# Kernel optimization log

Measured on AMD Instinct MI355X. Metric: run time of the kernel, lower is better.

Reference implementation:

```python
import jax, jax.numpy as jnp
import numpy as np
from jax import lax

DIM = 384; D_STATE = 16; D_CONV = 4; EXPAND = 2
D_INNER = DIM * EXPAND            # 768
DT_RANK = (DIM + 15) // 16        # 24
B_, H_, W_, Z_ = 2, 16, 16, 16
L_ = H_ * W_ * Z_                 # 4096 tokens
NSL = 16                          # num_slices_small

def silu(v):
    return v * jax.nn.sigmoid(v)

def setup_inputs() -> dict:
    keys = iter(jax.random.split(jax.random.key(0), 64))
    def rnd(shape, s=0.02):
        return jax.random.normal(next(keys), shape, jnp.float32) * s
    inp = {"x": jax.random.normal(next(keys), (B_, DIM, H_, W_, Z_), jnp.float32)}
    inp["ln_g"] = jnp.ones((DIM,), jnp.float32); inp["ln_b"] = jnp.zeros((DIM,), jnp.float32)
    inp["in_w"] = rnd((2 * D_INNER, DIM)); inp["out_w"] = rnd((DIM, D_INNER))
    # standard S4D-real init: A_log = log([1..d_state]) per inner channel
    A0 = jnp.log(jnp.tile(jnp.arange(1, D_STATE + 1, dtype=jnp.float32), (D_INNER, 1)))
    for t in ("f", "b", "s"):   # forward / backward / slice-wise scan branches
        inp["convw_" + t] = rnd((D_INNER, 1, D_CONV), 0.1)
        inp["convb_" + t] = jnp.zeros((D_INNER,), jnp.float32)
        inp["xpw_" + t] = rnd((DT_RANK + 2 * D_STATE, D_INNER))
        inp["dtw_" + t] = rnd((D_INNER, DT_RANK), 0.1)
        inp["dtb_" + t] = jnp.full((D_INNER,), -4.6, jnp.float32)  # softplus ~= 0.01
        inp["Alog_" + t] = A0
        inp["Dp_" + t] = jnp.ones((D_INNER,), jnp.float32)
    for i in (1, 2, 3, 4):      # FeatureFusion3D 1x1x1 convs == channel GEMMs
        inp["c%dw" % i] = rnd((DIM, DIM)); inp["c%db" % i] = jnp.zeros((DIM,), jnp.float32)
    return inp

def _ssm_scan(dt, Bc, Cc, u, A, Dp):
    # dt,u: [B,L,di]; Bc,Cc: [B,L,ds]; A: [di,ds]  -- selective scan, time-major lax.scan
    def step(h, inp):
        dt_t, B_t, C_t, u_t = inp                      # [B,di],[B,ds],[B,ds],[B,di]
        h = h * jnp.exp(dt_t[..., None] * A) + (dt_t * u_t)[..., None] * B_t[:, None, :]
        return h, jnp.einsum('bds,bs->bd', h, C_t)
    xs = (dt.swapaxes(0, 1), Bc.swapaxes(0, 1), Cc.swapaxes(0, 1), u.swapaxes(0, 1))
    h0 = jnp.zeros((dt.shape[0], A.shape[0], A.shape[1]), dt.dtype)
    _, ys = lax.scan(step, h0, xs)                     # ys: [L,B,di]
    return ys.swapaxes(0, 1) + u * Dp

def _branch(xi, convw, convb, xpw, dtw, dtb, Alog, Dp):
    # xi: [B,L,di]; causal depthwise conv1d + SiLU, then input-dependent dt/B/C, then scan
    xc = lax.conv_general_dilated(xi.swapaxes(1, 2), convw, (1,), [(D_CONV - 1, 0)],
                                  feature_group_count=D_INNER,
                                  dimension_numbers=('NCH', 'OIH', 'NCH'))
    xc = silu((xc + convb[None, :, None]).swapaxes(1, 2))      # [B,L,di]
    dbl = xc @ xpw.T                                           # [B,L,dt_rank+2*ds]
    dt_r, Bc, Cc = jnp.split(dbl, [DT_RANK, DT_RANK + D_STATE], axis=-1)
    dt = jax.nn.softplus(dt_r @ dtw.T + dtb)                   # [B,L,di]
    return _ssm_scan(dt, Bc, Cc, xc, -jnp.exp(Alog), Dp)

def _forward(x, ln_g, ln_b, in_w, out_w,
             convw_f, convb_f, xpw_f, dtw_f, dtb_f, Alog_f, Dp_f,
             convw_b, convb_b, xpw_b, dtw_b, dtb_b, Alog_b, Dp_b,
             convw_s, convb_s, xpw_s, dtw_s, dtb_s, Alog_s, Dp_s,
             c1w, c1b, c2w, c2b, c3w, c3b, c4w, c4b):
    B, C = x.shape[:2]; img = x.shape[2:]; L = img[0] * img[1] * img[2]
    xf = x.reshape(B, C, L).swapaxes(1, 2)                     # [B,L,C]
    mu = xf.mean(-1, keepdims=True)
    var = xf.var(-1, keepdims=True)
    xn = (xf - mu) * lax.rsqrt(var + 1e-5) * ln_g + ln_b       # LayerNorm
    xz = xn @ in_w.T                                           # [B,L,2*di]
    xi, z = jnp.split(xz, 2, axis=-1)
    # slice-wise reordering for the v3 inter-slice scan (static permutation)
    perm = np.arange(L).reshape(NSL, L // NSL).T.reshape(-1)
    inv = np.argsort(perm)
    y_f = _branch(xi, convw_f, convb_f, xpw_f, dtw_f, dtb_f, Alog_f, Dp_f)
    y_b = jnp.flip(_branch(jnp.flip(xi, 1), convw_b, convb_b, xpw_b, dtw_b, dtb_b, Alog_b, Dp_b), 1)
    y_s = _branch(xi[:, perm], convw_s, convb_s, xpw_s, dtw_s, dtb_s, Alog_s, Dp_s)[:, inv]
    g = silu(z)
    x_sq = ((y_f + y_b) * g) @ out_w.T                         # bidirectional branch output
    x_sl = (y_s * g) @ out_w.T                                 # slice-scan branch output
    out_sq = x_sq.swapaxes(1, 2).reshape(B, C, *img)
    out_sl = x_sl.swapaxes(1, 2).reshape(B, C, *img)
    out = out_sq + out_sl
    # FeatureFusion3D: global branch (avgpool + two 1x1x1) + spatial branch (two 1x1x1)
    gp = out.mean(axis=(2, 3, 4))                              # [B,C]
    gf = jax.nn.relu(gp @ c1w.T + c1b) @ c2w.T + c2b
    sp = jax.nn.relu(jnp.einsum('oc,bcxyz->boxyz', c3w, out) + c3b[None, :, None, None, None])
    sp = jnp.einsum('oc,bcxyz->boxyz', c4w, sp) + c4b[None, :, None, None, None]
    wff = jax.nn.sigmoid(gf[:, :, None, None, None] + sp)
    return out_sq * wff + (1.0 - wff) * out_sl + x             # gated combine + residual

def reference(x, ln_g, ln_b, in_w, out_w,
              convw_f, convb_f, xpw_f, dtw_f, dtb_f, Alog_f, Dp_f,
              convw_b, convb_b, xpw_b, dtw_b, dtb_b, Alog_b, Dp_b,
              convw_s, convb_s, xpw_s, dtw_s, dtb_s, Alog_s, Dp_s,
              c1w, c1b, c2w, c2b, c3w, c3b, c4w, c4b):
    return _forward(x, ln_g, ln_b, in_w, out_w,
                    convw_f, convb_f, xpw_f, dtw_f, dtb_f, Alog_f, Dp_f,
                    convw_b, convb_b, xpw_b, dtw_b, dtb_b, Alog_b, Dp_b,
                    convw_s, convb_s, xpw_s, dtw_s, dtb_s, Alog_s, Dp_s,
                    c1w, c1b, c2w, c2b, c3w, c3b, c4w, c4b)
```

## Files before the change

kernel.cpp:

```cpp
#include <hip/hip_runtime.h>
#include <math.h>

#define LT     4096
#define CDIM   384
#define DI     768
#define DS     16
#define NBATCH 2
#define NCHK   128
#define CHSZ   32
#define NSUP   16
#define MROWS  (NBATCH*LT)
#define NPROJ  800

using short8 = __attribute__((ext_vector_type(8))) short;
using f32x4  = __attribute__((ext_vector_type(4))) float;

__device__ __forceinline__ int posmap(int branch, int t){
  if (branch == 0) return t;
  if (branch == 1) return LT - 1 - t;
  return ((t & 15) << 8) | (t >> 4);
}

__device__ __forceinline__ short f2bf(float f){
  union { float f; unsigned u; } v; v.f = f;
  unsigned r = (v.u + 0x7FFFu + ((v.u >> 16) & 1u)) >> 16;
  return (short)r;
}
__device__ __forceinline__ float bf2f(short s){
  union { unsigned u; float f; } v; v.u = ((unsigned)(unsigned short)s) << 16;
  return v.f;
}
__device__ __forceinline__ float softplusf(float x){
  return (x > 20.f) ? x : __logf(1.f + __expf(x));
}

__global__ __launch_bounds__(256) void cvt_bf16(const float* __restrict__ src,
    short* __restrict__ dst, int n)
{
  const int i = blockIdx.x*256 + threadIdx.x;
  if (i < n) dst[i] = f2bf(src[i]);
}

#define LNPAD 69
__global__ __launch_bounds__(256) void ln_kernel(const float* __restrict__ x,
    const float* __restrict__ gam, const float* __restrict__ bet,
    short* __restrict__ xn)
{
  __shared__ float tile[64 * LNPAD];
  __shared__ float redS[16][16][4];
  __shared__ float redS2[16][16][4];
  __shared__ float muL[64], rsL[64];
  const int b  = blockIdx.y;
  const int l0 = blockIdx.x * 64;
  const int t  = threadIdx.x;
  const int g  = t >> 4, lf = t & 15;
  float s[4] = {0,0,0,0}, s2[4] = {0,0,0,0};
  for (int cc = 0; cc < 24; cc++){
    const int c = cc*16 + g;
    const float4 v = *(const float4*)&x[((size_t)b*CDIM + c)*LT + l0 + lf*4];
    s[0]+=v.x; s[1]+=v.y; s[2]+=v.z; s[3]+=v.w;
    s2[0]+=v.x*v.x; s2[1]+=v.y*v.y; s2[2]+=v.z*v.z; s2[3]+=v.w*v.w;
  }
#pragma unroll
  for (int j = 0; j < 4; j++){ redS[g][lf][j] = s[j]; redS2[g][lf][j] = s2[j]; }
  __syncthreads();
  if (t < 64){
    float ss = 0.f, ss2 = 0.f;
#pragma unroll
    for (int gg = 0; gg < 16; gg++){
      ss  += redS[gg][t>>2][t&3];
      ss2 += redS2[gg][t>>2][t&3];
    }
    const float mu  = ss * (1.f/CDIM);
    const float var = ss2 * (1.f/CDIM) - mu*mu;
    muL[t] = mu; rsL[t] = rsqrtf(var + 1e-5f);
  }
  __syncthreads();
  for (int chunk = 0; chunk < 6; chunk++){
    const int c0 = chunk*64;
#pragma unroll
    for (int p = 0; p < 4; p++){
      const int cl = p*16 + g;
      const float4 v = *(const float4*)&x[((size_t)b*CDIM + c0 + cl)*LT + l0 + lf*4];
      tile[cl*LNPAD + lf*4 + 0] = v.x;
      tile[cl*LNPAD + lf*4 + 1] = v.y;
      tile[cl*LNPAD + lf*4 + 2] = v.z;
      tile[cl*LNPAD + lf*4 + 3] = v.w;
    }
    __syncthreads();
    const int c_w = t & 63;
    const float gv = gam[c0 + c_w], bv = bet[c0 + c_w];
#pragma unroll
    for (int p = 0; p < 16; p++){
      const int l = p*4 + (t >> 6);
      xn[((size_t)b*LT + l0 + l)*CDIM + c0 + c_w] =
          f2bf((tile[c_w*LNPAD + l] - muL[l])*rsL[l]*gv + bv);
    }
    __syncthreads();
  }
}

__global__ __launch_bounds__(256) void mkwcat(const float* __restrict__ xpw,
    const float* __restrict__ dtw, short* __restrict__ wcat)
{
  const int k = blockIdx.x*256 + threadIdx.x;
  const int o = blockIdx.y;
  if (o < 32){
    wcat[(size_t)o*DI + k] = f2bf(xpw[(size_t)(24 + o)*DI + k]);
  } else {
    const float* dr = dtw + (size_t)(o - 32)*24;
    float acc = 0.f;
#pragma unroll
    for (int j = 0; j < 24; j++) acc += dr[j] * xpw[(size_t)j*DI + k];
    wcat[(size_t)o*DI + k] = f2bf(acc);
  }
}

template<int ACT>
__global__ __launch_bounds__(256) void gemm_bf16(const short* __restrict__ A, int lda,
    const short* __restrict__ Bw, int ldb, const float* __restrict__ bias,
    void* __restrict__ C, void* __restrict__ C2, int ldc,
    int M, int N, int K)
{
  __shared__ __align__(16) short As[64*40];
  __shared__ __align__(16) short Bs[64*40];
  const int tid  = threadIdx.x;
  const int m0   = blockIdx.x*64, n0 = blockIdx.y*64;
  const int w    = tid >> 6, lane = tid & 63;
  const int wm   = (w >> 1)*32, wn = (w & 1)*32;
  const int lrow = lane & 15, lko = (lane >> 4)*8;
  const int lr   = tid >> 2, lkc = (tid & 3)*8;

  const short* Aptr = A + (size_t)(m0 + lr)*lda + lkc;
  const bool   bok  = (n0 + lr) < N;
  const short* Bptr = Bw + (size_t)(n0 + lr)*ldb + lkc;

  f32x4 acc[2][2];
#pragma unroll
  for (int i = 0; i < 2; i++)
#pragma unroll
    for (int j = 0; j < 2; j++) acc[i][j] = (f32x4){0.f,0.f,0.f,0.f};

  short8 pa = *(const short8*)Aptr;
  short8 pb = bok ? *(const short8*)Bptr : (short8){0,0,0,0,0,0,0,0};

  for (int k0 = 0; k0 < K; k0 += 32){
    *(short8*)&As[lr*40 + lkc] = pa;
    *(short8*)&Bs[lr*40 + lkc] = pb;
    __syncthreads();
    if (k0 + 32 < K){
      pa = *(const short8*)(Aptr + k0 + 32);
      pb = bok ? *(const short8*)(Bptr + k0 + 32) : (short8){0,0,0,0,0,0,0,0};
    }
    const short8 a0 = *(const short8*)&As[(wm +      lrow)*40 + lko];
    const short8 a1 = *(const short8*)&As[(wm + 16 + lrow)*40 + lko];
    const short8 b0 = *(const short8*)&Bs[(wn +      lrow)*40 + lko];
    const short8 b1 = *(const short8*)&Bs[(wn + 16 + lrow)*40 + lko];
    acc[0][0] = __builtin_amdgcn_mfma_f32_16x16x32_bf16(a0, b0, acc[0][0], 0,0,0);
    acc[0][1] = __builtin_amdgcn_mfma_f32_16x16x32_bf16(a0, b1, acc[0][1], 0,0,0);
    acc[1][0] = __builtin_amdgcn_mfma_f32_16x16x32_bf16(a1, b0, acc[1][0], 0,0,0);
    acc[1][1] = __builtin_amdgcn_mfma_f32_16x16x32_bf16(a1, b1, acc[1][1], 0,0,0);
    __syncthreads();
  }
#pragma unroll
  for (int mi = 0; mi < 2; mi++){
#pragma unroll
    for (int nj = 0; nj < 2; nj++){
      const int n = n0 + wn + nj*16 + lrow;
      if (n >= N) continue;
      const float bv = ((ACT == 0 || ACT == 8 || ACT == 9) && bias) ? bias[n] : 0.f;
#pragma unroll
      for (int reg = 0; reg < 4; reg++){
        const int m = m0 + wm + mi*16 + (lane >> 4)*4 + reg;
        float v = acc[mi][nj][reg] + bv;
        if (ACT == 0){
          ((float*)C)[(size_t)m*ldc + n] = v;
        } else if (ACT == 4){
          if (n < DI) ((short*)C)[(size_t)m*DI + n] = f2bf(v);
          else ((short*)C2)[(size_t)m*DI + (n - DI)] = f2bf(v / (1.f + __expf(-v)));
        } else if (ACT == 6){
          if (n < 32) ((float*)C)[(size_t)m*32 + n] = v;
          else ((short*)C2)[(size_t)m*DI + (n - 32)] =
                   f2bf(softplusf(v + bias[n - 32]));
        } else if (ACT == 7){
          ((short*)C)[(size_t)m*ldc + n] = f2bf(v);
        } else if (ACT == 8){
          ((short*)C)[(size_t)m*ldc + n] = f2bf(fmaxf(v, 0.f));
        } else if (ACT == 9){
          ((short*)C)[(size_t)m*ldc + n] = f2bf(v);
        }
      }
    }
  }
}

__global__ __launch_bounds__(256) void conv_branch(const short* __restrict__ xi,
    const float* __restrict__ w, const float* __restrict__ bias,
    short* __restrict__ xc, int branch)
{
  const int d  = blockIdx.x*256 + threadIdx.x;
  const int t0 = blockIdx.y*4;
  const int b  = blockIdx.z;
  const float w0 = w[d*4+0], w1 = w[d*4+1], w2 = w[d*4+2], w3 = w[d*4+3];
  const float bv = bias[d];
  float xm3 = 0.f, xm2 = 0.f, xm1 = 0.f;
  if (t0 > 0){
    xm3 = bf2f(xi[((size_t)b*LT + posmap(branch, t0-3))*DI + d]);
    xm2 = bf2f(xi[((size_t)b*LT + posmap(branch, t0-2))*DI + d]);
    xm1 = bf2f(xi[((size_t)b*LT + posmap(branch, t0-1))*DI + d]);
  }
#pragma unroll
  for (int i = 0; i < 4; i++){
    const int t = t0 + i;
    const float cur = bf2f(xi[((size_t)b*LT + posmap(branch, t))*DI + d]);
    const float acc = bv + w0*xm3 + w1*xm2 + w2*xm1 + w3*cur;
    const float sg = 1.f / (1.f + __expf(-acc));
    xc[((size_t)b*LT + t)*DI + d] = f2bf(acc * sg);
    xm3 = xm2; xm2 = xm1; xm1 = cur;
  }
}


__global__ __launch_bounds__(256) void scan_hs(const short* __restrict__ xc,
    const float* __restrict__ dbl32, const short* __restrict__ dtv_g,
    const float* __restrict__ Alog,
    float* __restrict__ hfin, float* __restrict__ sdt_buf)
{
  __shared__ float bS[CHSZ*16];
  __shared__ short dS[CHSZ*64];
  __shared__ short uS[CHSZ*64];
  const int t  = threadIdx.x;
  const int q  = t & 3;
  const int dl = t >> 2;
  const int d0 = blockIdx.x*64;
  const int d  = d0 + dl;
  const int c  = blockIdx.y;
  const int b  = blockIdx.z;
  const size_t row0 = (size_t)b*LT + c*CHSZ;
  {
    if (t < 128){
      const int r = t >> 2, c4 = t & 3;
      *(float4*)&bS[r*16 + c4*4] = *(const float4*)&dbl32[(row0 + r)*32 + c4*4];
    }
    const int r = t >> 3, c8 = t & 7;
    *(short8*)&dS[r*64 + c8*8] = *(const short8*)&dtv_g[(row0 + r)*DI + d0 + c8*8];
    *(short8*)&uS[r*64 + c8*8] = *(const short8*)&xc[(row0 + r)*DI + d0 + c8*8];
  }
  float Ad[4];
#pragma unroll
  for (int j = 0; j < 4; j++) Ad[j] = -__expf(Alog[d*DS + q*4 + j]);
  __syncthreads();
  float h[4] = {0.f,0.f,0.f,0.f};
  float sdt = 0.f;
#pragma unroll 4
  for (int tl = 0; tl < CHSZ; tl++){
    const float dtv = bf2f(dS[tl*64 + dl]);
    const float u   = bf2f(uS[tl*64 + dl]);
    const f32x4 Bv = *(const f32x4*)&bS[tl*16 + q*4];
    const float du = dtv * u;
#pragma unroll
    for (int j = 0; j < 4; j++)
      h[j] = h[j]*__expf(dtv*Ad[j]) + du*Bv[j];
    sdt += dtv;
  }
  const size_t off = ((size_t)b*NCHK + c)*DI + d;
  *(f32x4*)&hfin[off*DS + q*4] = (f32x4){h[0], h[1], h[2], h[3]};
  if (q == 0) sdt_buf[off] = sdt;
}

__global__ __launch_bounds__(256) void scan_b1(const float* __restrict__ hfin,
    const float* __restrict__ sdt_buf, const float* __restrict__ Alog,
    float* __restrict__ PS, float* __restrict__ QS)
{
  const int t = threadIdx.x;
  const int q = t & 3;
  const int d = blockIdx.x*64 + (t >> 2);
  const int s = blockIdx.y;
  const int b = blockIdx.z;
  float Ad[4];
#pragma unroll
  for (int j = 0; j < 4; j++) Ad[j] = -__expf(Alog[d*DS + q*4 + j]);
  float P[4] = {1.f,1.f,1.f,1.f}, Q[4] = {0.f,0.f,0.f,0.f};
  for (int k = 0; k < NCHK/NSUP; k++){
    const size_t off = ((size_t)b*NCHK + s*(NCHK/NSUP) + k)*DI + d;
    const float sd = sdt_buf[off];
    const f32x4 hf = *(const f32x4*)&hfin[off*DS + q*4];
#pragma unroll
    for (int j = 0; j < 4; j++){
      const float e = __expf(Ad[j]*sd);
      Q[j] = hf[j] + e*Q[j];
      P[j] *= e;
    }
  }
  const size_t so = ((size_t)b*NSUP + s)*DI + d;
  *(f32x4*)&PS[so*DS + q*4] = (f32x4){P[0], P[1], P[2], P[3]};
  *(f32x4*)&QS[so*DS + q*4] = (f32x4){Q[0], Q[1], Q[2], Q[3]};
}

__global__ __launch_bounds__(256) void scan_b2(const float* __restrict__ PS,
    float* __restrict__ QS)
{
  const int t = threadIdx.x;
  const int q = t & 3;
  const int d = blockIdx.x*64 + (t >> 2);
  const int b = blockIdx.y;
  float cr[4] = {0.f,0.f,0.f,0.f};
  for (int s = 0; s < NSUP; s++){
    const size_t so = ((size_t)b*NSUP + s)*DI + d;
    const f32x4 P = *(const f32x4*)&PS[so*DS + q*4];
    const f32x4 Q = *(const f32x4*)&QS[so*DS + q*4];
    *(f32x4*)&QS[so*DS + q*4] = (f32x4){cr[0], cr[1], cr[2], cr[3]};
#pragma unroll
    for (int j = 0; j < 4; j++) cr[j] = Q[j] + P[j]*cr[j];
  }
}

__global__ __launch_bounds__(256) void scan_b3(float* __restrict__ hfin,
    const float* __restrict__ sdt_buf, const float* __restrict__ Alog,
    const float* __restrict__ QS)
{
  const int t = threadIdx.x;
  const int q = t & 3;
  const int d = blockIdx.x*64 + (t >> 2);
  const int s = blockIdx.y;
  const int b = blockIdx.z;
  float Ad[4];
#pragma unroll
  for (int j = 0; j < 4; j++) Ad[j] = -__expf(Alog[d*DS + q*4 + j]);
  const size_t so = ((size_t)b*NSUP + s)*DI + d;
  const f32x4 sc = *(const f32x4*)&QS[so*DS + q*4];
  float cr[4] = {sc[0], sc[1], sc[2], sc[3]};
  for (int k = 0; k < NCHK/NSUP; k++){
    const size_t off = ((size_t)b*NCHK + s*(NCHK/NSUP) + k)*DI + d;
    const float sd = sdt_buf[off];
    const f32x4 hf = *(const f32x4*)&hfin[off*DS + q*4];
    *(f32x4*)&hfin[off*DS + q*4] = (f32x4){cr[0], cr[1], cr[2], cr[3]};
#pragma unroll
    for (int j = 0; j < 4; j++) cr[j] = hf[j] + __expf(Ad[j]*sd)*cr[j];
  }
}

__global__ __launch_bounds__(256) void scan_y(const short* __restrict__ xc,
    const float* __restrict__ dbl32, const short* __restrict__ dtv_g,
    const float* __restrict__ Alog, const float* __restrict__ Dp,
    const float* __restrict__ carry, const short* __restrict__ gate,
    short* __restrict__ y, int branch, int mode)
{
  __shared__ float bS[CHSZ*32];
  __shared__ short dS[CHSZ*64];
  __shared__ short uS[CHSZ*64];
  const int t  = threadIdx.x;
  const int q  = t & 3;
  const int dl = t >> 2;
  const int d0 = blockIdx.x*64;
  const int d  = d0 + dl;
  const int c  = blockIdx.y;
  const int b  = blockIdx.z;
  const size_t row0 = (size_t)b*LT + c*CHSZ;
  {
    const int r4 = t >> 3, c4 = t & 7;
    *(float4*)&bS[r4*32 + c4*4] = *(const float4*)&dbl32[(row0 + r4)*32 + c4*4];
    const int r = t >> 3, c8 = t & 7;
    *(short8*)&dS[r*64 + c8*8] = *(const short8*)&dtv_g[(row0 + r)*DI + d0 + c8*8];
    *(short8*)&uS[r*64 + c8*8] = *(const short8*)&xc[(row0 + r)*DI + d0 + c8*8];
  }
  float Ad[4];
#pragma unroll
  for (int j = 0; j < 4; j++) Ad[j] = -__expf(Alog[d*DS + q*4 + j]);
  const float Dpv = Dp[d];
  const size_t coff = (((size_t)b*NCHK + c)*DI + d)*DS;
  float h[4];
  {
    const f32x4 cv = *(const f32x4*)&carry[coff + q*4];
    h[0] = cv[0]; h[1] = cv[1]; h[2] = cv[2]; h[3] = cv[3];
  }
  __syncthreads();
#pragma unroll 4
  for (int tl = 0; tl < CHSZ; tl++){
    const float dtv = bf2f(dS[tl*64 + dl]);
    const float u   = bf2f(uS[tl*64 + dl]);
    const f32x4 Bv = *(const f32x4*)&bS[tl*32 + q*4];
    const f32x4 Cv = *(const f32x4*)&bS[tl*32 + 16 + q*4];
    const float du = dtv * u;
    float yv = 0.f;
#pragma unroll
    for (int j = 0; j < 4; j++){
      h[j] = h[j]*__expf(dtv*Ad[j]) + du*Bv[j];
      yv  += h[j]*Cv[j];
    }
    yv += __shfl_xor(yv, 1);
    yv += __shfl_xor(yv, 2);
    if (q == 0){
      const float out = yv + u*Dpv;
      const size_t oidx = ((size_t)b*LT + posmap(branch, c*CHSZ + tl))*DI + d;
      if (mode == 0)      y[oidx] = f2bf(out);
      else if (mode == 1) y[oidx] = f2bf((bf2f(y[oidx]) + out) * bf2f(gate[oidx]));
      else                y[oidx] = f2bf(out * bf2f(gate[oidx]));
    }
  }
}

__global__ __launch_bounds__(384) void add_gp(const short* __restrict__ xsq,
    const short* __restrict__ xsl, short* __restrict__ osum,
    float* __restrict__ gpp)
{
  const int c = threadIdx.x;
  const int p = blockIdx.x;
  const int b = blockIdx.y;
  const int l0 = p * (LT/128);
  float s = 0.f;
  for (int i = 0; i < LT/128; i++){
    const size_t idx = ((size_t)b*LT + l0 + i)*CDIM + c;
    const float v = bf2f(xsq[idx]) + bf2f(xsl[idx]);
    osum[idx] = f2bf(v);
    s += v;
  }
  gpp[((size_t)b*128 + p)*CDIM + c] = s;
}

__global__ __launch_bounds__(384) void gpl_kernel(const float* __restrict__ gpp,
    float* __restrict__ gpl)
{
  const int c = threadIdx.x, b = blockIdx.x;
  float s = 0.f;
#pragma unroll 8
  for (int p = 0; p < 128; p++) s += gpp[((size_t)b*128 + p)*CDIM + c];
  gpl[b*CDIM + c] = s * (1.f/LT);
}

template<int RELU>
__global__ __launch_bounds__(256) void gf_mm(const float* __restrict__ in,
    const float* __restrict__ w, const float* __restrict__ bias,
    float* __restrict__ out)
{
  __shared__ float inS[CDIM];
  const int t = threadIdx.x, b = blockIdx.y;
  const int o = blockIdx.x*64 + (t >> 2), lane = t & 3;
  for (int i = t; i < CDIM; i += 256) inS[i] = in[b*CDIM + i];
  __syncthreads();
  const float* wr = w + (size_t)o*CDIM + lane*96;
  const float* gr = inS + lane*96;
  float s = 0.f;
#pragma unroll
  for (int i = 0; i < 24; i++){
    const float4 wv = *(const float4*)&wr[i*4];
    const float4 gv = *(const float4*)&gr[i*4];
    s += wv.x*gv.x + wv.y*gv.y + wv.z*gv.z + wv.w*gv.w;
  }
  s += __shfl_xor(s, 1);
  s += __shfl_xor(s, 2);
  if (lane == 0){
    float v = s + bias[o];
    if (RELU) v = fmaxf(v, 0.f);
    out[b*CDIM + o] = v;
  }
}

#define FTPAD 68
__global__ __launch_bounds__(256) void final_kernel(const short* __restrict__ xsq,
    const short* __restrict__ xsl, const short* __restrict__ sp2,
    const float* __restrict__ gf, const float* __restrict__ x,
    float* __restrict__ out)
{
  __shared__ float vt[64 * FTPAD];
  __shared__ float gfl[64];
  const int b  = blockIdx.z;
  const int c0 = blockIdx.y * 64;
  const int l0 = blockIdx.x * 64;
  const int t  = threadIdx.x;
  if (t < 64) gfl[t] = gf[b*CDIM + c0 + t];
  __syncthreads();
  const int lf = t & 15;
#pragma unroll
  for (int p = 0; p < 4; p++){
    const int ll = (t >> 4) + p*16;
    const size_t base = ((size_t)b*LT + l0 + ll)*CDIM + c0 + lf*4;
    const short4 a4 = *(const short4*)&xsq[base];
    const short4 s4 = *(const short4*)&xsl[base];
    const short4 c4 = *(const short4*)&sp2[base];
    float4 v;
    { const float wf = 1.f/(1.f+__expf(-(gfl[lf*4+0] + bf2f(c4.x))));
      v.x = bf2f(a4.x)*wf + (1.f-wf)*bf2f(s4.x); }
    { const float wf = 1.f/(1.f+__expf(-(gfl[lf*4+1] + bf2f(c4.y))));
      v.y = bf2f(a4.y)*wf + (1.f-wf)*bf2f(s4.y); }
    { const float wf = 1.f/(1.f+__expf(-(gfl[lf*4+2] + bf2f(c4.z))));
      v.z = bf2f(a4.z)*wf + (1.f-wf)*bf2f(s4.z); }
    { const float wf = 1.f/(1.f+__expf(-(gfl[lf*4+3] + bf2f(c4.w))));
      v.w = bf2f(a4.w)*wf + (1.f-wf)*bf2f(s4.w); }
    *(float4*)&vt[ll*FTPAD + lf*4] = v;
  }
  __syncthreads();
#pragma unroll
  for (int q = 0; q < 4; q++){
    const int c_w = (t >> 4) + q*16;
    const size_t oi = ((size_t)b*CDIM + c0 + c_w)*LT + l0 + lf*4;
    const float4 xv = *(const float4*)&x[oi];
    float4 o;
    o.x = vt[(lf*4+0)*FTPAD + c_w] + xv.x;
    o.y = vt[(lf*4+1)*FTPAD + c_w] + xv.y;
    o.z = vt[(lf*4+2)*FTPAD + c_w] + xv.z;
    o.w = vt[(lf*4+3)*FTPAD + c_w] + xv.w;
    *(float4*)&out[oi] = o;
  }
}

extern "C" void kernel_launch(void* const* d_in, const int* in_sizes, int n_in,
                              void* d_out, int out_size, void* d_ws, size_t ws_size,
                              hipStream_t stream)
{
  (void)in_sizes; (void)n_in; (void)out_size;
  const float* X    = (const float*)d_in[0];
  const float* LNG  = (const float*)d_in[1];
  const float* LNB  = (const float*)d_in[2];
  const float* INW  = (const float*)d_in[3];
  const float* OUTW = (const float*)d_in[4];
  const float *CONVW[3], *CONVB[3], *XPW[3], *DTW[3], *DTB[3], *ALOG[3], *DPP[3];
  for (int t = 0; t < 3; t++){
    int base = 5 + 7*t;
    CONVW[t] = (const float*)d_in[base + 0];
    CONVB[t] = (const float*)d_in[base + 1];
    XPW[t]   = (const float*)d_in[base + 2];
    DTW[t]   = (const float*)d_in[base + 3];
    DTB[t]   = (const float*)d_in[base + 4];
    ALOG[t]  = (const float*)d_in[base + 5];
    DPP[t]   = (const float*)d_in[base + 6];
  }
  const float* C1W = (const float*)d_in[26];
  const float* C1B = (const float*)d_in[27];
  const float* C2W = (const float*)d_in[28];
  const float* C2B = (const float*)d_in[29];
  const float* C3W = (const float*)d_in[30];
  const float* C3B = (const float*)d_in[31];
  const float* C4W = (const float*)d_in[32];
  const float* C4B = (const float*)d_in[33];

  const size_t SCR_SZ = 10835968;
  size_t off = 0;
  float* ws    = (float*)d_ws;
  float* SCR   = ws + off; off += SCR_SZ;
  short* XI    = (short*)(ws + off); off += (size_t)MROWS*DI/2;
  short* GATE  = (short*)(ws + off); off += (size_t)MROWS*DI/2;
  short* Y     = (short*)(ws + off); off += (size_t)MROWS*DI/2;
  short* XSL   = (short*)(ws + off); off += (size_t)MROWS*CDIM/2;
  short* INWB  = (short*)(ws + off); off += (size_t)2*DI*CDIM/2;
  short* OUTWB = (short*)(ws + off); off += (size_t)CDIM*DI/2;
  short* C3WB  = (short*)(ws + off); off += (size_t)CDIM*CDIM/2;
  short* C4WB  = (short*)(ws + off); off += (size_t)CDIM*CDIM/2;
  const size_t need_bytes = off * sizeof(float);
  if (ws_size < need_bytes) return;

  short* XN    = (short*)SCR;
  short* XC    = (short*)SCR;
  float* DBLB  = SCR + 3145728;
  float* HFIN  = SCR + 3407872;
  float* SDT   = SCR + 6553600;
  short* WCATB = (short*)(SCR + 6750208);
  short* DTBUF = (short*)(SCR + 6903808);
  float* PS    = SCR + 10049536;
  float* QS    = SCR + 10442752;
  short* OSUM = (short*)SCR;
  short* SP1  = (short*)(SCR + 1572864);
  short* SP2  = (short*)(SCR + 3145728);
  float* GPP  = SCR + 6291456;
  float* GPL  = SCR + 6389760;
  float* T1   = SCR + 6390528;
  float* GF   = SCR + 6391296;
  short* XSQ  = XI;
  float* DOUT = (float*)d_out;

  cvt_bf16<<<dim3((2*DI*CDIM + 255)/256), 256, 0, stream>>>(INW, INWB, 2*DI*CDIM);
  cvt_bf16<<<dim3((CDIM*DI + 255)/256), 256, 0, stream>>>(OUTW, OUTWB, CDIM*DI);
  cvt_bf16<<<dim3((CDIM*CDIM + 255)/256), 256, 0, stream>>>(C3W, C3WB, CDIM*CDIM);
  cvt_bf16<<<dim3((CDIM*CDIM + 255)/256), 256, 0, stream>>>(C4W, C4WB, CDIM*CDIM);
  ln_kernel<<<dim3(LT/64, NBATCH), 256, 0, stream>>>(X, LNG, LNB, XN);
  gemm_bf16<4><<<dim3(128, 24), 256, 0, stream>>>(XN, CDIM, INWB, CDIM, nullptr,
      XI, GATE, 0, MROWS, 2*DI, CDIM);
  const int order[3] = {2, 0, 1};
  for (int oi_ = 0; oi_ < 3; oi_++){
    const int t = order[oi_];
    conv_branch<<<dim3(3, LT/4, NBATCH), 256, 0, stream>>>(XI, CONVW[t], CONVB[t], XC, t);
    mkwcat<<<dim3(3, NPROJ), 256, 0, stream>>>(XPW[t], DTW[t], WCATB);
    gemm_bf16<6><<<dim3(128, 13), 256, 0, stream>>>(XC, DI, WCATB, DI, DTB[t],
        DBLB, DTBUF, 0, MROWS, NPROJ, DI);
    scan_hs<<<dim3(DI/64, NCHK, NBATCH), 256, 0, stream>>>(XC, DBLB, DTBUF,
                                                           ALOG[t], HFIN, SDT);
    scan_b1<<<dim3(DI/64, NSUP, NBATCH), 256, 0, stream>>>(HFIN, SDT, ALOG[t], PS, QS);
    scan_b2<<<dim3(DI/64, NBATCH), 256, 0, stream>>>(PS, QS);
    scan_b3<<<dim3(DI/64, NSUP, NBATCH), 256, 0, stream>>>(HFIN, SDT, ALOG[t], QS);
    const int mode = (t == 2) ? 2 : (t == 1) ? 1 : 0;
    scan_y<<<dim3(DI/64, NCHK, NBATCH), 256, 0, stream>>>(XC, DBLB, DTBUF,
                                                          ALOG[t], DPP[t], HFIN,
                                                          GATE, Y, t, mode);
    if (t == 2){
      gemm_bf16<7><<<dim3(128, 6), 256, 0, stream>>>(Y, DI, OUTWB, DI, nullptr,
          XSL, nullptr, CDIM, MROWS, CDIM, DI);
    } else if (t == 1){
      gemm_bf16<7><<<dim3(128, 6), 256, 0, stream>>>(Y, DI, OUTWB, DI, nullptr,
          XSQ, nullptr, CDIM, MROWS, CDIM, DI);
    }
  }
  add_gp<<<dim3(128, NBATCH), 384, 0, stream>>>(XSQ, XSL, OSUM, GPP);
  gpl_kernel<<<dim3(NBATCH), 384, 0, stream>>>(GPP, GPL);
  gf_mm<1><<<dim3(CDIM/64, NBATCH), 256, 0, stream>>>(GPL, C1W, C1B, T1);
  gf_mm<0><<<dim3(CDIM/64, NBATCH), 256, 0, stream>>>(T1, C2W, C2B, GF);
  gemm_bf16<8><<<dim3(128, 6), 256, 0, stream>>>(OSUM, CDIM, C3WB, CDIM, C3B,
      SP1, nullptr, CDIM, MROWS, CDIM, CDIM);
  gemm_bf16<9><<<dim3(128, 6), 256, 0, stream>>>(SP1, CDIM, C4WB, CDIM, C4B,
      SP2, nullptr, CDIM, MROWS, CDIM, CDIM);
  final_kernel<<<dim3(LT/64, CDIM/64, NBATCH), 256, 0, stream>>>(XSQ, XSL, SP2,
                                                                 GF, X, DOUT);
}
```

Before: 490.7 us.

## Fuse local scan with output, add carry correction pass via cumulative dt

```diff
diff --git a/kernel.cpp b/kernel.cpp
--- a/kernel.cpp
+++ b/kernel.cpp
@@ -220,135 +220,16 @@
   }
 }
 
-
-__global__ __launch_bounds__(256) void scan_hs(const short* __restrict__ xc,
-    const float* __restrict__ dbl32, const short* __restrict__ dtv_g,
-    const float* __restrict__ Alog,
-    float* __restrict__ hfin, float* __restrict__ sdt_buf)
-{
-  __shared__ float bS[CHSZ*16];
-  __shared__ short dS[CHSZ*64];
-  __shared__ short uS[CHSZ*64];
-  const int t  = threadIdx.x;
-  const int q  = t & 3;
-  const int dl = t >> 2;
-  const int d0 = blockIdx.x*64;
-  const int d  = d0 + dl;
-  const int c  = blockIdx.y;
-  const int b  = blockIdx.z;
-  const size_t row0 = (size_t)b*LT + c*CHSZ;
-  {
-    if (t < 128){
-      const int r = t >> 2, c4 = t & 3;
-      *(float4*)&bS[r*16 + c4*4] = *(const float4*)&dbl32[(row0 + r)*32 + c4*4];
-    }
-    const int r = t >> 3, c8 = t & 7;
-    *(short8*)&dS[r*64 + c8*8] = *(const short8*)&dtv_g[(row0 + r)*DI + d0 + c8*8];
-    *(short8*)&uS[r*64 + c8*8] = *(const short8*)&xc[(row0 + r)*DI + d0 + c8*8];
-  }
-  float Ad[4];
-#pragma unroll
-  for (int j = 0; j < 4; j++) Ad[j] = -__expf(Alog[d*DS + q*4 + j]);
-  __syncthreads();
-  float h[4] = {0.f,0.f,0.f,0.f};
-  float sdt = 0.f;
-#pragma unroll 4
-  for (int tl = 0; tl < CHSZ; tl++){
-    const float dtv = bf2f(dS[tl*64 + dl]);
-    const float u   = bf2f(uS[tl*64 + dl]);
-    const f32x4 Bv = *(const f32x4*)&bS[tl*16 + q*4];
-    const float du = dtv * u;
-#pragma unroll
-    for (int j = 0; j < 4; j++)
-      h[j] = h[j]*__expf(dtv*Ad[j]) + du*Bv[j];
-    sdt += dtv;
-  }
-  const size_t off = ((size_t)b*NCHK + c)*DI + d;
-  *(f32x4*)&hfin[off*DS + q*4] = (f32x4){h[0], h[1], h[2], h[3]};
-  if (q == 0) sdt_buf[off] = sdt;
-}
-
-__global__ __launch_bounds__(256) void scan_b1(const float* __restrict__ hfin,
-    const float* __restrict__ sdt_buf, const float* __restrict__ Alog,
-    float* __restrict__ PS, float* __restrict__ QS)
-{
-  const int t = threadIdx.x;
-  const int q = t & 3;
-  const int d = blockIdx.x*64 + (t >> 2);
-  const int s = blockIdx.y;
-  const int b = blockIdx.z;
-  float Ad[4];
-#pragma unroll
-  for (int j = 0; j < 4; j++) Ad[j] = -__expf(Alog[d*DS + q*4 + j]);
-  float P[4] = {1.f,1.f,1.f,1.f}, Q[4] = {0.f,0.f,0.f,0.f};
-  for (int k = 0; k < NCHK/NSUP; k++){
-    const size_t off = ((size_t)b*NCHK + s*(NCHK/NSUP) + k)*DI + d;
-    const float sd = sdt_buf[off];
-    const f32x4 hf = *(const f32x4*)&hfin[off*DS + q*4];
-#pragma unroll
-    for (int j = 0; j < 4; j++){
-      const float e = __expf(Ad[j]*sd);
-      Q[j] = hf[j] + e*Q[j];
-      P[j] *= e;
-    }
-  }
-  const size_t so = ((size_t)b*NSUP + s)*DI + d;
-  *(f32x4*)&PS[so*DS + q*4] = (f32x4){P[0], P[1], P[2], P[3]};
-  *(f32x4*)&QS[so*DS + q*4] = (f32x4){Q[0], Q[1], Q[2], Q[3]};
-}
-
-__global__ __launch_bounds__(256) void scan_b2(const float* __restrict__ PS,
-    float* __restrict__ QS)
-{
-  const int t = threadIdx.x;
-  const int q = t & 3;
-  const int d = blockIdx.x*64 + (t >> 2);
-  const int b = blockIdx.y;
-  float cr[4] = {0.f,0.f,0.f,0.f};
-  for (int s = 0; s < NSUP; s++){
-    const size_t so = ((size_t)b*NSUP + s)*DI + d;
-    const f32x4 P = *(const f32x4*)&PS[so*DS + q*4];
-    const f32x4 Q = *(const f32x4*)&QS[so*DS + q*4];
-    *(f32x4*)&QS[so*DS + q*4] = (f32x4){cr[0], cr[1], cr[2], cr[3]};
-#pragma unroll
-    for (int j = 0; j < 4; j++) cr[j] = Q[j] + P[j]*cr[j];
-  }
-}
-
-__global__ __launch_bounds__(256) void scan_b3(float* __restrict__ hfin,
-    const float* __restrict__ sdt_buf, const float* __restrict__ Alog,
-    const float* __restrict__ QS)
-{
-  const int t = threadIdx.x;
-  const int q = t & 3;
-  const int d = blockIdx.x*64 + (t >> 2);
-  const int s = blockIdx.y;
-  const int b = blockIdx.z;
-  float Ad[4];
-#pragma unroll
-  for (int j = 0; j < 4; j++) Ad[j] = -__expf(Alog[d*DS + q*4 + j]);
-  const size_t so = ((size_t)b*NSUP + s)*DI + d;
-  const f32x4 sc = *(const f32x4*)&QS[so*DS + q*4];
-  float cr[4] = {sc[0], sc[1], sc[2], sc[3]};
-  for (int k = 0; k < NCHK/NSUP; k++){
-    const size_t off = ((size_t)b*NCHK + s*(NCHK/NSUP) + k)*DI + d;
-    const float sd = sdt_buf[off];
-    const f32x4 hf = *(const f32x4*)&hfin[off*DS + q*4];
-    *(f32x4*)&hfin[off*DS + q*4] = (f32x4){cr[0], cr[1], cr[2], cr[3]};
-#pragma unroll
-    for (int j = 0; j < 4; j++) cr[j] = hf[j] + __expf(Ad[j]*sd)*cr[j];
-  }
-}
-
-__global__ __launch_bounds__(256) void scan_y(const short* __restrict__ xc,
+__global__ __launch_bounds__(256) void scan_local(const short* __restrict__ xc,
     const float* __restrict__ dbl32, const short* __restrict__ dtv_g,
     const float* __restrict__ Alog, const float* __restrict__ Dp,
-    const float* __restrict__ carry, const short* __restrict__ gate,
-    short* __restrict__ y, int branch, int mode)
-{
-  __shared__ float bS[CHSZ*32];
-  __shared__ short dS[CHSZ*64];
-  __shared__ short uS[CHSZ*64];
+    short* __restrict__ y, short* __restrict__ cumdt_g,
+    float* __restrict__ hfin, float* __restrict__ sdt_buf,
+    int branch, int accumA)
+{
+  __shared__ float    bS[CHSZ*32];
+  __shared__ unsigned udS[CHSZ*64];
+  __shared__ short    cS[CHSZ*64];
   const int t  = threadIdx.x;
   const int q  = t & 3;
   const int dl = t >> 2;
@@ -361,24 +242,32 @@
     const int r4 = t >> 3, c4 = t & 7;
     *(float4*)&bS[r4*32 + c4*4] = *(const float4*)&dbl32[(row0 + r4)*32 + c4*4];
     const int r = t >> 3, c8 = t & 7;
-    *(short8*)&dS[r*64 + c8*8] = *(const short8*)&dtv_g[(row0 + r)*DI + d0 + c8*8];
-    *(short8*)&uS[r*64 + c8*8] = *(const short8*)&xc[(row0 + r)*DI + d0 + c8*8];
+    const short8 d8 = *(const short8*)&dtv_g[(row0 + r)*DI + d0 + c8*8];
+    const short8 u8 = *(const short8*)&xc[(row0 + r)*DI + d0 + c8*8];
+    uint4 p0, p1;
+    p0.x = ((unsigned)(unsigned short)u8[0] << 16) | (unsigned)(unsigned short)d8[0];
+    p0.y = ((unsigned)(unsigned short)u8[1] << 16) | (unsigned)(unsigned short)d8[1];
+    p0.z = ((unsigned)(unsigned short)u8[2] << 16) | (unsigned)(unsigned short)d8[2];
+    p0.w = ((unsigned)(unsigned short)u8[3] << 16) | (unsigned)(unsigned short)d8[3];
+    p1.x = ((unsigned)(unsigned short)u8[4] << 16) | (unsigned)(unsigned short)d8[4];
+    p1.y = ((unsigned)(unsigned short)u8[5] << 16) | (unsigned)(unsigned short)d8[5];
+    p1.z = ((unsigned)(unsigned short)u8[6] << 16) | (unsigned)(unsigned short)d8[6];
+    p1.w = ((unsigned)(unsigned short)u8[7] << 16) | (unsigned)(unsigned short)d8[7];
+    *(uint4*)&udS[r*64 + c8*8]     = p0;
+    *(uint4*)&udS[r*64 + c8*8 + 4] = p1;
   }
   float Ad[4];
 #pragma unroll
   for (int j = 0; j < 4; j++) Ad[j] = -__expf(Alog[d*DS + q*4 + j]);
   const float Dpv = Dp[d];
-  const size_t coff = (((size_t)b*NCHK + c)*DI + d)*DS;
-  float h[4];
-  {
-    const f32x4 cv = *(const f32x4*)&carry[coff + q*4];
-    h[0] = cv[0]; h[1] = cv[1]; h[2] = cv[2]; h[3] = cv[3];
-  }
-  __syncthreads();
+  __syncthreads();
+  float h[4] = {0.f,0.f,0.f,0.f};
+  float sdt = 0.f;
 #pragma unroll 4
   for (int tl = 0; tl < CHSZ; tl++){
-    const float dtv = bf2f(dS[tl*64 + dl]);
-    const float u   = bf2f(uS[tl*64 + dl]);
+    const unsigned wv = udS[tl*64 + dl];
+    const float dtv = bf2f((short)(wv & 0xFFFFu));
+    const float u   = bf2f((short)(wv >> 16));
     const f32x4 Bv = *(const f32x4*)&bS[tl*32 + q*4];
     const f32x4 Cv = *(const f32x4*)&bS[tl*32 + 16 + q*4];
     const float du = dtv * u;
@@ -388,14 +277,143 @@
       h[j] = h[j]*__expf(dtv*Ad[j]) + du*Bv[j];
       yv  += h[j]*Cv[j];
     }
+    sdt += dtv;
+    if (q == 0) cS[tl*64 + dl] = f2bf(sdt);
     yv += __shfl_xor(yv, 1);
     yv += __shfl_xor(yv, 2);
     if (q == 0){
       const float out = yv + u*Dpv;
       const size_t oidx = ((size_t)b*LT + posmap(branch, c*CHSZ + tl))*DI + d;
-      if (mode == 0)      y[oidx] = f2bf(out);
-      else if (mode == 1) y[oidx] = f2bf((bf2f(y[oidx]) + out) * bf2f(gate[oidx]));
-      else                y[oidx] = f2bf(out * bf2f(gate[oidx]));
+      if (accumA) y[oidx] = f2bf(bf2f(y[oidx]) + out);
+      else        y[oidx] = f2bf(out);
+    }
+  }
+  const size_t off = ((size_t)b*NCHK + c)*DI + d;
+  *(f32x4*)&hfin[off*DS + q*4] = (f32x4){h[0], h[1], h[2], h[3]};
+  if (q == 0) sdt_buf[off] = sdt;
+  __syncthreads();
+  {
+    const int r = t >> 3, c8 = t & 7;
+    *(short8*)&cumdt_g[(row0 + r)*DI + d0 + c8*8] = *(const short8*)&cS[r*64 + c8*8];
+  }
+}
+
+__global__ __launch_bounds__(256) void scan_b1(const float* __restrict__ hfin,
+    const float* __restrict__ sdt_buf, const float* __restrict__ Alog,
+    float* __restrict__ PS, float* __restrict__ QS)
+{
+  const int t = threadIdx.x;
+  const int q = t & 3;
+  const int d = blockIdx.x*64 + (t >> 2);
+  const int s = blockIdx.y;
+  const int b = blockIdx.z;
+  float Ad[4];
+#pragma unroll
+  for (int j = 0; j < 4; j++) Ad[j] = -__expf(Alog[d*DS + q*4 + j]);
+  float P[4] = {1.f,1.f,1.f,1.f}, Q[4] = {0.f,0.f,0.f,0.f};
+  for (int k = 0; k < NCHK/NSUP; k++){
+    const size_t off = ((size_t)b*NCHK + s*(NCHK/NSUP) + k)*DI + d;
+    const float sd = sdt_buf[off];
+    const f32x4 hf = *(const f32x4*)&hfin[off*DS + q*4];
+#pragma unroll
+    for (int j = 0; j < 4; j++){
+      const float e = __expf(Ad[j]*sd);
+      Q[j] = hf[j] + e*Q[j];
+      P[j] *= e;
+    }
+  }
+  const size_t so = ((size_t)b*NSUP + s)*DI + d;
+  *(f32x4*)&PS[so*DS + q*4] = (f32x4){P[0], P[1], P[2], P[3]};
+  *(f32x4*)&QS[so*DS + q*4] = (f32x4){Q[0], Q[1], Q[2], Q[3]};
+}
+
+__global__ __launch_bounds__(256) void scan_b2(const float* __restrict__ PS,
+    float* __restrict__ QS)
+{
+  const int t = threadIdx.x;
+  const int q = t & 3;
+  const int d = blockIdx.x*64 + (t >> 2);
+  const int b = blockIdx.y;
+  float cr[4] = {0.f,0.f,0.f,0.f};
+  for (int s = 0; s < NSUP; s++){
+    const size_t so = ((size_t)b*NSUP + s)*DI + d;
+    const f32x4 P = *(const f32x4*)&PS[so*DS + q*4];
+    const f32x4 Q = *(const f32x4*)&QS[so*DS + q*4];
+    *(f32x4*)&QS[so*DS + q*4] = (f32x4){cr[0], cr[1], cr[2], cr[3]};
+#pragma unroll
+    for (int j = 0; j < 4; j++) cr[j] = Q[j] + P[j]*cr[j];
+  }
+}
+
+__global__ __launch_bounds__(256) void scan_b3(float* __restrict__ hfin,
+    const float* __restrict__ sdt_buf, const float* __restrict__ Alog,
+    const float* __restrict__ QS)
+{
+  const int t = threadIdx.x;
+  const int q = t & 3;
+  const int d = blockIdx.x*64 + (t >> 2);
+  const int s = blockIdx.y;
+  const int b = blockIdx.z;
+  float Ad[4];
+#pragma unroll
+  for (int j = 0; j < 4; j++) Ad[j] = -__expf(Alog[d*DS + q*4 + j]);
+  const size_t so = ((size_t)b*NSUP + s)*DI + d;
+  const f32x4 sc = *(const f32x4*)&QS[so*DS + q*4];
+  float cr[4] = {sc[0], sc[1], sc[2], sc[3]};
+  for (int k = 0; k < NCHK/NSUP; k++){
+    const size_t off = ((size_t)b*NCHK + s*(NCHK/NSUP) + k)*DI + d;
+    const float sd = sdt_buf[off];
+    const f32x4 hf = *(const f32x4*)&hfin[off*DS + q*4];
+    *(f32x4*)&hfin[off*DS + q*4] = (f32x4){cr[0], cr[1], cr[2], cr[3]};
+#pragma unroll
+    for (int j = 0; j < 4; j++) cr[j] = hf[j] + __expf(Ad[j]*sd)*cr[j];
+  }
+}
+
+__global__ __launch_bounds__(256) void scan_corr(const float* __restrict__ dbl32,
+    const short* __restrict__ cumdt_g, const float* __restrict__ Alog,
+    const float* __restrict__ carry, const short* __restrict__ gate,
+    short* __restrict__ y, int branch, int gateC)
+{
+  __shared__ float cC[CHSZ*16];
+  __shared__ short cdS[CHSZ*64];
+  const int t  = threadIdx.x;
+  const int q  = t & 3;
+  const int dl = t >> 2;
+  const int d0 = blockIdx.x*64;
+  const int d  = d0 + dl;
+  const int c  = blockIdx.y;
+  const int b  = blockIdx.z;
+  const size_t row0 = (size_t)b*LT + c*CHSZ;
+  {
+    if (t < 128){
+      const int r = t >> 2, c4 = t & 3;
+      *(float4*)&cC[r*16 + c4*4] = *(const float4*)&dbl32[(row0 + r)*32 + 16 + c4*4];
+    }
+    const int r = t >> 3, c8 = t & 7;
+    *(short8*)&cdS[r*64 + c8*8] = *(const short8*)&cumdt_g[(row0 + r)*DI + d0 + c8*8];
+  }
+  float Ad[4];
+#pragma unroll
+  for (int j = 0; j < 4; j++) Ad[j] = -__expf(Alog[d*DS + q*4 + j]);
+  const size_t coff = (((size_t)b*NCHK + c)*DI + d)*DS;
+  const f32x4 cv = *(const f32x4*)&carry[coff + q*4];
+  __syncthreads();
+#pragma unroll 4
+  for (int tl = 0; tl < CHSZ; tl++){
+    const float cd = bf2f(cdS[tl*64 + dl]);
+    const f32x4 Cv = *(const f32x4*)&cC[tl*16 + q*4];
+    float corr = 0.f;
+#pragma unroll
+    for (int j = 0; j < 4; j++)
+      corr += Cv[j]*cv[j]*__expf(Ad[j]*cd);
+    corr += __shfl_xor(corr, 1);
+    corr += __shfl_xor(corr, 2);
+    if (q == 0){
+      const size_t oidx = ((size_t)b*LT + posmap(branch, c*CHSZ + tl))*DI + d;
+      float val = bf2f(y[oidx]) + corr;
+      if (gateC) val *= bf2f(gate[oidx]);
+      y[oidx] = f2bf(val);
     }
   }
 }
@@ -534,7 +552,7 @@
   const float* C4W = (const float*)d_in[32];
   const float* C4B = (const float*)d_in[33];
 
-  const size_t SCR_SZ = 10835968;
+  const size_t SCR_SZ = 12408832;
   size_t off = 0;
   float* ws    = (float*)d_ws;
   float* SCR   = ws + off; off += SCR_SZ;
@@ -558,6 +576,7 @@
   short* DTBUF = (short*)(SCR + 6903808);
   float* PS    = SCR + 10049536;
   float* QS    = SCR + 10442752;
+  short* CUMDT = (short*)(SCR + 10835968);
   short* OSUM = (short*)SCR;
   short* SP1  = (short*)(SCR + 1572864);
   short* SP2  = (short*)(SCR + 3145728);
@@ -582,15 +601,13 @@
     mkwcat<<<dim3(3, NPROJ), 256, 0, stream>>>(XPW[t], DTW[t], WCATB);
     gemm_bf16<6><<<dim3(128, 13), 256, 0, stream>>>(XC, DI, WCATB, DI, DTB[t],
         DBLB, DTBUF, 0, MROWS, NPROJ, DI);
-    scan_hs<<<dim3(DI/64, NCHK, NBATCH), 256, 0, stream>>>(XC, DBLB, DTBUF,
-                                                           ALOG[t], HFIN, SDT);
+    scan_local<<<dim3(DI/64, NCHK, NBATCH), 256, 0, stream>>>(XC, DBLB, DTBUF,
+        ALOG[t], DPP[t], Y, CUMDT, HFIN, SDT, t, (t == 1) ? 1 : 0);
     scan_b1<<<dim3(DI/64, NSUP, NBATCH), 256, 0, stream>>>(HFIN, SDT, ALOG[t], PS, QS);
     scan_b2<<<dim3(DI/64, NBATCH), 256, 0, stream>>>(PS, QS);
     scan_b3<<<dim3(DI/64, NSUP, NBATCH), 256, 0, stream>>>(HFIN, SDT, ALOG[t], QS);
-    const int mode = (t == 2) ? 2 : (t == 1) ? 1 : 0;
-    scan_y<<<dim3(DI/64, NCHK, NBATCH), 256, 0, stream>>>(XC, DBLB, DTBUF,
-                                                          ALOG[t], DPP[t], HFIN,
-                                                          GATE, Y, t, mode);
+    scan_corr<<<dim3(DI/64, NCHK, NBATCH), 256, 0, stream>>>(DBLB, CUMDT, ALOG[t],
+        HFIN, GATE, Y, t, (t == 0) ? 0 : 1);
     if (t == 2){
       gemm_bf16<7><<<dim3(128, 6), 256, 0, stream>>>(Y, DI, OUTWB, DI, nullptr,
           XSL, nullptr, CDIM, MROWS, CDIM, DI);
```

After: 559.2 us. 1.14x slower.
